# Kernel optimization log

Hardware: AMD Instinct MI355X
Metric: run time of the kernel (lower is better)

Reference implementation:

```python
import jax, jax.numpy as jnp
import numpy as np

NQ = 8  # qubits per circuit (= d_k = n_qubits_ffn)
# Fixed realization of tq.RandomLayer(n_ops=8): 6 parametric rotations + 2 CNOTs
OPS = [("ry", 0), ("rx", 3), ("rz", 5), ("cx", (1, 4)), ("ry", 6), ("rx", 2), ("cx", (0, 7)), ("rz", 4)]
_CNOT = jnp.asarray(np.array([[1,0,0,0],[0,1,0,0],[0,0,0,1],[0,0,1,0]], dtype=np.complex64).reshape(2,2,2,2))
# signs[i, w] = +1 if bit of wire w in basis index i is 0, else -1 (PauliZ eigenvalue)
_idx = np.arange(2 ** NQ)
_bits = (_idx[:, None] >> (NQ - 1 - np.arange(NQ))) & 1
SIGNS = jnp.asarray((1 - 2 * _bits).astype(np.float32))

def _rot(kind, t):
    c = jnp.cos(t / 2).astype(jnp.complex64)
    s = jnp.sin(t / 2).astype(jnp.complex64)
    z = jnp.zeros_like(c)
    if kind == "rx":
        return jnp.stack([jnp.stack([c, -1j * s]), jnp.stack([-1j * s, c])])
    if kind == "ry":
        return jnp.stack([jnp.stack([c, -s]), jnp.stack([s, c])])
    tc = t.astype(jnp.complex64)
    return jnp.stack([jnp.stack([jnp.exp(-1j * tc / 2), z]), jnp.stack([z, jnp.exp(1j * tc / 2)])])

def _apply1(state, U, w):
    st = jnp.tensordot(U, state, axes=((1,), (w + 1,)))
    return jnp.moveaxis(st, 0, w + 1)

def _apply2(state, c, t):  # CNOT, requires c < t (true for OPS)
    st = jnp.tensordot(_CNOT, state, axes=((2, 3), (c + 1, t + 1)))
    return jnp.moveaxis(st, (0, 1), (c + 1, t + 1))

def qcircuit(angles, thetas):
    """angles: [N, NQ] data angles (RX encoding); thetas: [6] gate params.
    Returns PauliZ expectations [N, NQ] (float32)."""
    N = angles.shape[0]
    c = jnp.cos(angles / 2)
    s = jnp.sin(angles / 2)
    amp = jnp.stack([c.astype(jnp.complex64), (-1j) * s.astype(jnp.complex64)], axis=-1)  # [N, NQ, 2]
    # RX-encoded product state |psi> = prod_w RX(x_w)|0>
    state = amp[:, 0]
    for w in range(1, NQ):
        state = state[..., None] * amp[:, w].reshape((N,) + (1,) * w + (2,))
    pi = 0
    for kind, arg in OPS:
        if kind == "cx":
            state = _apply2(state, *arg)
        else:
            state = _apply1(state, _rot(kind, thetas[pi]), arg)
            pi += 1
    probs = jnp.abs(state.reshape(N, -1)) ** 2  # [N, 2^NQ]
    return probs @ SIGNS  # [N, NQ]

def _ln(x, g, b, eps=1e-5):
    m = x.mean(-1, keepdims=True)
    v = ((x - m) ** 2).mean(-1, keepdims=True)
    return (x - m) / jnp.sqrt(v + eps) * g + b

def setup_inputs() -> dict:
    key = jax.random.key(0)
    ks = jax.random.split(key, 8)
    B, S, E, FF = 4, 1024, 64, 256
    return {
        "x": jax.random.normal(ks[0], (B, S, E), dtype=jnp.float32),
        "attn_theta": jax.random.uniform(ks[1], (6,), dtype=jnp.float32, maxval=2 * np.pi),
        "Wc": jax.random.normal(ks[2], (E, E), dtype=jnp.float32) * 0.1,
        "bc": jnp.zeros((E,), jnp.float32),
        "g1": jnp.ones((E,), jnp.float32),
        "beta1": jnp.zeros((E,), jnp.float32),
        "ffn_theta": jax.random.uniform(ks[3], (6,), dtype=jnp.float32, maxval=2 * np.pi),
        "W1": jax.random.normal(ks[4], (NQ, FF), dtype=jnp.float32) * 0.3,
        "b1": jnp.zeros((FF,), jnp.float32),
        "W2": jax.random.normal(ks[5], (FF, E), dtype=jnp.float32) * 0.06,
        "b2": jnp.zeros((E,), jnp.float32),
        "g2": jnp.ones((E,), jnp.float32),
        "beta2": jnp.zeros((E,), jnp.float32),
    }

def reference(x, attn_theta, Wc, bc, g1, beta1, ffn_theta, W1, b1, W2, b2, g2, beta2):
    B, S, E = x.shape
    dk = NQ  # d_k = embed_dim // num_heads = 8
    # --- quantum multi-head attention (same qlayer shared across heads -> vectorize) ---
    q = qcircuit(x.reshape(B * S * (E // dk), dk), attn_theta)  # [B*S*H, dk]
    attn = q.reshape(B, S, E) @ Wc + bc
    y = _ln(x + attn, g1, beta1)
    # --- quantum FFN: encoder uses first NQ features of each token ---
    qf = qcircuit(y.reshape(B * S, E)[:, :NQ], ffn_theta)  # [B*S, NQ]
    h = jax.nn.relu(qf @ W1 + b1)
    ffn = (h @ W2 + b2).reshape(B, S, E)
    return _ln(y + ffn, g2, beta2)
```

## Files before the change

### kernel.cpp

```cpp
#include <hip/hip_runtime.h>


typedef _Float16 h2f  __attribute__((ext_vector_type(2)));
typedef _Float16 f16x8 __attribute__((ext_vector_type(8)));
typedef float    f32x4 __attribute__((ext_vector_type(4)));

__device__ __forceinline__ int pk(float a, float b) {
    return __builtin_bit_cast(int, __builtin_amdgcn_cvt_pkrtz(a, b));
}
__device__ __forceinline__ float fdot2i(int a, int b, float c) {
    return __builtin_amdgcn_fdot2(__builtin_bit_cast(h2f, a),
                                  __builtin_bit_cast(h2f, b), c, false);
}
__device__ __forceinline__ float rl_f(float v, int l) {
    return __int_as_float(__builtin_amdgcn_readlane(__float_as_int(v), l));
}
__device__ __forceinline__ int rl_i(int v, int l) {
    return __builtin_amdgcn_readlane(v, l);
}
__device__ __forceinline__ void wave_sum2(float& a, float& b) {
#pragma unroll
    for (int m = 32; m > 0; m >>= 1) {
        a += __shfl_xor(a, m, 64);
        b += __shfl_xor(b, m, 64);
    }
}

__global__ __launch_bounds__(512, 2)
void qtb_fused8(const float* __restrict__ x,
                const float* __restrict__ th_a,
                const float* __restrict__ Wc,
                const float* __restrict__ bc,
                const float* __restrict__ g1,
                const float* __restrict__ be1,
                const float* __restrict__ th_f,
                const float* __restrict__ W1,
                const float* __restrict__ b1,
                const float* __restrict__ W2,
                const float* __restrict__ b2,
                const float* __restrict__ g2,
                const float* __restrict__ be2,
                float* __restrict__ out)
{
    __shared__ __align__(16) int2      sWc[16 * 64];
    __shared__ __align__(16) int4      sW1[256];
    __shared__ __align__(16) _Float16  sW2t[64][264];
    __shared__ __align__(16) _Float16  sH[16][264];
    __shared__ __align__(16) float     sO[16][66];

    const int tid  = threadIdx.x;
    const int lane = tid & 63;
    const int wv   = tid >> 6;
    const int w    = lane & 7;
    const int gb   = lane & ~7;
    const int tok0 = (blockIdx.x * 8 + wv) * 2;

    {
        int k0 = (tid & 31) * 8;
        int e0 = (tid >> 5) * 4;
        float4 r[8];
#pragma unroll
        for (int i = 0; i < 8; ++i)
            r[i] = *(const float4*)&W2[(k0 + i) * 64 + e0];
        const float* f = (const float*)r;
#pragma unroll
        for (int j = 0; j < 4; ++j) {
            int4 wj = make_int4(pk(f[0 * 4 + j], f[1 * 4 + j]),
                                pk(f[2 * 4 + j], f[3 * 4 + j]),
                                pk(f[4 * 4 + j], f[5 * 4 + j]),
                                pk(f[6 * 4 + j], f[7 * 4 + j]));
            *(int4*)&sW2t[e0 + j][k0] = wj;
        }
    }
    if (tid < 256) {
        int q2 = tid >> 4;
        int e0 = (tid & 15) * 4;
        const float* b = Wc + e0;
        float4 r0 = *(const float4*)&b[(2 * q2     ) * 64];
        float4 r1 = *(const float4*)&b[(2 * q2 +  1) * 64];
        float4 r2 = *(const float4*)&b[(2 * q2 + 32) * 64];
        float4 r3 = *(const float4*)&b[(2 * q2 + 33) * 64];
        int4* dst = (int4*)&sWc[q2 * 64 + e0];
        dst[0] = make_int4(pk(r0.x, r2.x), pk(r1.x, r3.x),
                           pk(r0.y, r2.y), pk(r1.y, r3.y));
        dst[1] = make_int4(pk(r0.z, r2.z), pk(r1.z, r3.z),
                           pk(r0.w, r2.w), pk(r1.w, r3.w));
    } else if (tid < 320) {
        int j0 = (tid - 256) * 4;
        float4 r[8];
#pragma unroll
        for (int k = 0; k < 8; ++k) r[k] = *(const float4*)&W1[k * 256 + j0];
        const float* f = (const float*)r;
        int4* dst = &sW1[j0];
#pragma unroll
        for (int j = 0; j < 4; ++j)
            dst[j] = make_int4(pk(f[0 * 4 + j], f[4 * 4 + j]),
                               pk(f[1 * 4 + j], f[5 * 4 + j]),
                               pk(f[2 * 4 + j], f[6 * 4 + j]),
                               pk(f[3 * 4 + j], f[7 * 4 + j]));
    }

    float xr[2];
#pragma unroll
    for (int t = 0; t < 2; ++t) xr[t] = x[(tok0 + t) * 64 + lane];

    const float C0a = __cosf(th_a[0]);
    const float T1a = th_a[1];
    const float C3a = __cosf(th_a[3]);
    const float T4a = th_a[4];
    const float C0f = __cosf(th_f[0]);
    const float T1f = th_f[1];
    const float C3f = __cosf(th_f[3]);
    const float T4f = th_f[4];

    const float bcL = bc[lane], g1L = g1[lane], be1L = be1[lane];
    const float b2L = b2[lane], g2L = g2[lane], be2L = be2[lane];
    float b1L[4];
#pragma unroll
    for (int r = 0; r < 4; ++r) b1L[r] = b1[r * 64 + lane];

    const float dA = (w == 2) ? T4a : ((w == 3) ? T1a : 0.0f);
    int zp[2];
#pragma unroll
    for (int t = 0; t < 2; ++t) {
        float c  = __cosf(xr[t] + dA);
        float c0 = __shfl(c, gb, 64);
        float c1 = __shfl(c, gb + 1, 64);
        float zz = c * ((w == 0) ? C0a : ((w == 6) ? C3a : 1.0f));
        if (w == 4) zz = c * c1;
        if (w == 7) zz = C0a * c0 * c;
        zp[t] = pk(zz, __shfl_xor(zz, 32, 64));
    }

    __syncthreads();

    float acc[2] = {bcL, bcL};
#pragma unroll 4
    for (int q2 = 0; q2 < 16; ++q2) {
        int2 wq = sWc[q2 * 64 + lane];
        int q = 2 * q2;
        acc[0] = fdot2i(rl_i(zp[0], q),     wq.x, acc[0]);
        acc[1] = fdot2i(rl_i(zp[1], q),     wq.x, acc[1]);
        acc[0] = fdot2i(rl_i(zp[0], q + 1), wq.y, acc[0]);
        acc[1] = fdot2i(rl_i(zp[1], q + 1), wq.y, acc[1]);
    }

    float y[2];
#pragma unroll
    for (int t = 0; t < 2; ++t) {
        float v = xr[t] + acc[t];
        float s = v, s2 = v * v;
        wave_sum2(s, s2);
        float m   = s * 0.015625f;
        float var = s2 * 0.015625f - m * m;
        y[t] = (v - m) * rsqrtf(var + 1e-5f) * g1L + be1L;
    }

    int4 w1q[4];
#pragma unroll
    for (int r = 0; r < 4; ++r) w1q[r] = sW1[r * 64 + lane];

    const float dF = (w == 2) ? T4f : ((w == 3) ? T1f : 0.0f);
#pragma unroll
    for (int t = 0; t < 2; ++t) {
        float cy = __cosf(y[t] + dF);
        float c0 = rl_f(cy, 0);
        float c1 = rl_f(cy, 1);
        float qz = cy * ((w == 0) ? C0f : ((w == 6) ? C3f : 1.0f));
        if (w == 4) qz = cy * c1;
        if (w == 7) qz = C0f * c0 * cy;
        int qp0 = pk(rl_f(qz, 0), rl_f(qz, 4));
        int qp1 = pk(rl_f(qz, 1), rl_f(qz, 5));
        int qp2 = pk(rl_f(qz, 2), rl_f(qz, 6));
        int qp3 = pk(rl_f(qz, 3), rl_f(qz, 7));
#pragma unroll
        for (int r = 0; r < 4; ++r) {
            float a = b1L[r];
            a = fdot2i(qp0, w1q[r].x, a);
            a = fdot2i(qp1, w1q[r].y, a);
            a = fdot2i(qp2, w1q[r].z, a);
            a = fdot2i(qp3, w1q[r].w, a);
            sH[wv * 2 + t][r * 64 + lane] = (_Float16)fmaxf(a, 0.0f);
        }
    }

    __syncthreads();

    if (wv < 4) {
        const int col = lane & 15;
        const int kg  = lane >> 4;
        f32x4 cacc = {0.0f, 0.0f, 0.0f, 0.0f};
#pragma unroll
        for (int ks = 0; ks < 8; ++ks) {
            f16x8 af = *(const f16x8*)&sH[col][ks * 32 + kg * 8];
            f16x8 bf = *(const f16x8*)&sW2t[wv * 16 + col][ks * 32 + kg * 8];
            cacc = __builtin_amdgcn_mfma_f32_16x16x32_f16(af, bf, cacc, 0, 0, 0);
        }
#pragma unroll
        for (int r = 0; r < 4; ++r)
            sO[kg * 4 + r][wv * 16 + col] = cacc[r];
    }

    __syncthreads();

#pragma unroll
    for (int t = 0; t < 2; ++t) {
        float v = y[t] + b2L + sO[wv * 2 + t][lane];
        float s = v, s2 = v * v;
        wave_sum2(s, s2);
        float m   = s * 0.015625f;
        float var = s2 * 0.015625f - m * m;
        out[(tok0 + t) * 64 + lane] = (v - m) * rsqrtf(var + 1e-5f) * g2L + be2L;
    }
}

extern "C" void kernel_launch(void* const* d_in, const int* in_sizes, int n_in,
                              void* d_out, int out_size, void* d_ws, size_t ws_size,
                              hipStream_t stream)
{
    const float* x   = (const float*)d_in[0];
    const float* at  = (const float*)d_in[1];
    const float* Wc  = (const float*)d_in[2];
    const float* bcp = (const float*)d_in[3];
    const float* g1  = (const float*)d_in[4];
    const float* be1 = (const float*)d_in[5];
    const float* ft  = (const float*)d_in[6];
    const float* W1  = (const float*)d_in[7];
    const float* b1  = (const float*)d_in[8];
    const float* W2  = (const float*)d_in[9];
    const float* b2  = (const float*)d_in[10];
    const float* g2  = (const float*)d_in[11];
    const float* be2 = (const float*)d_in[12];
    float* out = (float*)d_out;

    qtb_fused8<<<256, 512, 0, stream>>>(x, at, Wc, bcp, g1, be1, ft,
                                        W1, b1, W2, b2, g2, be2, out);
}
```

Before: 11.58 us.

## Compute attention projection with MFMA and prefetch W2 fragments on idle waves

The per-lane readlane/fdot2 loop for the Wc projection is replaced by a 16x16x32 f16 MFMA over a transposed Wc tile in shared memory. Quantum Z outputs are staged through shared memory for this, which adds a barrier. Waves 4-7 now preload their W2 B-fragments into registers while waves 0-3 do the attention MFMA, and later those same waves run the FFN MFMA. The result is an extra sync and shared round trip in exchange for less scalar dot-product work, at the cost of higher register pressure.

```diff
diff --git a/kernel.cpp b/kernel.cpp
--- a/kernel.cpp
+++ b/kernel.cpp
@@ -1,7 +1,7 @@
 #include <hip/hip_runtime.h>
 
 
-typedef _Float16 h2f  __attribute__((ext_vector_type(2)));
+typedef _Float16 h2f   __attribute__((ext_vector_type(2)));
 typedef _Float16 f16x8 __attribute__((ext_vector_type(8)));
 typedef float    f32x4 __attribute__((ext_vector_type(4)));
 
@@ -15,9 +15,6 @@
 __device__ __forceinline__ float rl_f(float v, int l) {
     return __int_as_float(__builtin_amdgcn_readlane(__float_as_int(v), l));
 }
-__device__ __forceinline__ int rl_i(int v, int l) {
-    return __builtin_amdgcn_readlane(v, l);
-}
 __device__ __forceinline__ void wave_sum2(float& a, float& b) {
 #pragma unroll
     for (int m = 32; m > 0; m >>= 1) {
@@ -27,7 +24,7 @@
 }
 
 __global__ __launch_bounds__(512, 2)
-void qtb_fused8(const float* __restrict__ x,
+void qtb_fused9(const float* __restrict__ x,
                 const float* __restrict__ th_a,
                 const float* __restrict__ Wc,
                 const float* __restrict__ bc,
@@ -42,9 +39,11 @@
                 const float* __restrict__ be2,
                 float* __restrict__ out)
 {
-    __shared__ __align__(16) int2      sWc[16 * 64];
+    __shared__ __align__(16) _Float16  sWct[64][72];
     __shared__ __align__(16) int4      sW1[256];
     __shared__ __align__(16) _Float16  sW2t[64][264];
+    __shared__ __align__(16) _Float16  sZ[16][72];
+    __shared__ __align__(16) float     sA[16][66];
     __shared__ __align__(16) _Float16  sH[16][264];
     __shared__ __align__(16) float     sO[16][66];
 
@@ -54,6 +53,7 @@
     const int w    = lane & 7;
     const int gb   = lane & ~7;
     const int tok0 = (blockIdx.x * 8 + wv) * 2;
+    const int tl   = wv * 2;
 
     {
         int k0 = (tid & 31) * 8;
@@ -64,40 +64,40 @@
             r[i] = *(const float4*)&W2[(k0 + i) * 64 + e0];
         const float* f = (const float*)r;
 #pragma unroll
-        for (int j = 0; j < 4; ++j) {
-            int4 wj = make_int4(pk(f[0 * 4 + j], f[1 * 4 + j]),
-                                pk(f[2 * 4 + j], f[3 * 4 + j]),
-                                pk(f[4 * 4 + j], f[5 * 4 + j]),
-                                pk(f[6 * 4 + j], f[7 * 4 + j]));
-            *(int4*)&sW2t[e0 + j][k0] = wj;
-        }
-    }
-    if (tid < 256) {
-        int q2 = tid >> 4;
-        int e0 = (tid & 15) * 4;
-        const float* b = Wc + e0;
-        float4 r0 = *(const float4*)&b[(2 * q2     ) * 64];
-        float4 r1 = *(const float4*)&b[(2 * q2 +  1) * 64];
-        float4 r2 = *(const float4*)&b[(2 * q2 + 32) * 64];
-        float4 r3 = *(const float4*)&b[(2 * q2 + 33) * 64];
-        int4* dst = (int4*)&sWc[q2 * 64 + e0];
-        dst[0] = make_int4(pk(r0.x, r2.x), pk(r1.x, r3.x),
-                           pk(r0.y, r2.y), pk(r1.y, r3.y));
-        dst[1] = make_int4(pk(r0.z, r2.z), pk(r1.z, r3.z),
-                           pk(r0.w, r2.w), pk(r1.w, r3.w));
-    } else if (tid < 320) {
-        int j0 = (tid - 256) * 4;
+        for (int j = 0; j < 4; ++j)
+            *(int4*)&sW2t[e0 + j][k0] =
+                make_int4(pk(f[0 * 4 + j], f[1 * 4 + j]),
+                          pk(f[2 * 4 + j], f[3 * 4 + j]),
+                          pk(f[4 * 4 + j], f[5 * 4 + j]),
+                          pk(f[6 * 4 + j], f[7 * 4 + j]));
+    }
+    if (tid < 128) {
+        int q0 = (tid & 7) * 8;
+        int e0 = (tid >> 3) * 4;
+        float4 r[8];
+#pragma unroll
+        for (int i = 0; i < 8; ++i)
+            r[i] = *(const float4*)&Wc[(q0 + i) * 64 + e0];
+        const float* f = (const float*)r;
+#pragma unroll
+        for (int j = 0; j < 4; ++j)
+            *(int4*)&sWct[e0 + j][q0] =
+                make_int4(pk(f[0 * 4 + j], f[1 * 4 + j]),
+                          pk(f[2 * 4 + j], f[3 * 4 + j]),
+                          pk(f[4 * 4 + j], f[5 * 4 + j]),
+                          pk(f[6 * 4 + j], f[7 * 4 + j]));
+    } else if (tid < 192) {
+        int j0 = (tid - 128) * 4;
         float4 r[8];
 #pragma unroll
         for (int k = 0; k < 8; ++k) r[k] = *(const float4*)&W1[k * 256 + j0];
         const float* f = (const float*)r;
-        int4* dst = &sW1[j0];
 #pragma unroll
         for (int j = 0; j < 4; ++j)
-            dst[j] = make_int4(pk(f[0 * 4 + j], f[4 * 4 + j]),
-                               pk(f[1 * 4 + j], f[5 * 4 + j]),
-                               pk(f[2 * 4 + j], f[6 * 4 + j]),
-                               pk(f[3 * 4 + j], f[7 * 4 + j]));
+            sW1[j0 + j] = make_int4(pk(f[0 * 4 + j], f[4 * 4 + j]),
+                                    pk(f[1 * 4 + j], f[5 * 4 + j]),
+                                    pk(f[2 * 4 + j], f[6 * 4 + j]),
+                                    pk(f[3 * 4 + j], f[7 * 4 + j]));
     }
 
     float xr[2];
@@ -120,7 +120,6 @@
     for (int r = 0; r < 4; ++r) b1L[r] = b1[r * 64 + lane];
 
     const float dA = (w == 2) ? T4a : ((w == 3) ? T1a : 0.0f);
-    int zp[2];
 #pragma unroll
     for (int t = 0; t < 2; ++t) {
         float c  = __cosf(xr[t] + dA);
@@ -129,26 +128,40 @@
         float zz = c * ((w == 0) ? C0a : ((w == 6) ? C3a : 1.0f));
         if (w == 4) zz = c * c1;
         if (w == 7) zz = C0a * c0 * c;
-        zp[t] = pk(zz, __shfl_xor(zz, 32, 64));
-    }
-
-    __syncthreads();
-
-    float acc[2] = {bcL, bcL};
-#pragma unroll 4
-    for (int q2 = 0; q2 < 16; ++q2) {
-        int2 wq = sWc[q2 * 64 + lane];
-        int q = 2 * q2;
-        acc[0] = fdot2i(rl_i(zp[0], q),     wq.x, acc[0]);
-        acc[1] = fdot2i(rl_i(zp[1], q),     wq.x, acc[1]);
-        acc[0] = fdot2i(rl_i(zp[0], q + 1), wq.y, acc[0]);
-        acc[1] = fdot2i(rl_i(zp[1], q + 1), wq.y, acc[1]);
-    }
+        sZ[tl + t][lane] = (_Float16)zz;
+    }
+
+    __syncthreads();
+
+    const int col = lane & 15;
+    const int kg  = lane >> 4;
+
+    f16x8 bf2[8];
+    if (wv >= 4) {
+#pragma unroll
+        for (int ks = 0; ks < 8; ++ks)
+            bf2[ks] = *(const f16x8*)&sW2t[(wv - 4) * 16 + col][ks * 32 + kg * 8];
+    }
+
+    if (wv < 4) {
+        f32x4 cacc = {0.0f, 0.0f, 0.0f, 0.0f};
+#pragma unroll
+        for (int ks = 0; ks < 2; ++ks) {
+            f16x8 af = *(const f16x8*)&sZ[col][ks * 32 + kg * 8];
+            f16x8 bf = *(const f16x8*)&sWct[wv * 16 + col][ks * 32 + kg * 8];
+            cacc = __builtin_amdgcn_mfma_f32_16x16x32_f16(af, bf, cacc, 0, 0, 0);
+        }
+#pragma unroll
+        for (int r = 0; r < 4; ++r)
+            sA[kg * 4 + r][wv * 16 + col] = cacc[r];
+    }
+
+    __syncthreads();
 
     float y[2];
 #pragma unroll
     for (int t = 0; t < 2; ++t) {
-        float v = xr[t] + acc[t];
+        float v = xr[t] + sA[tl + t][lane] + bcL;
         float s = v, s2 = v * v;
         wave_sum2(s, s2);
         float m   = s * 0.015625f;
@@ -180,32 +193,29 @@
             a = fdot2i(qp1, w1q[r].y, a);
             a = fdot2i(qp2, w1q[r].z, a);
             a = fdot2i(qp3, w1q[r].w, a);
-            sH[wv * 2 + t][r * 64 + lane] = (_Float16)fmaxf(a, 0.0f);
+            sH[tl + t][r * 64 + lane] = (_Float16)fmaxf(a, 0.0f);
         }
     }
 
     __syncthreads();
 
-    if (wv < 4) {
-        const int col = lane & 15;
-        const int kg  = lane >> 4;
+    if (wv >= 4) {
         f32x4 cacc = {0.0f, 0.0f, 0.0f, 0.0f};
 #pragma unroll
         for (int ks = 0; ks < 8; ++ks) {
             f16x8 af = *(const f16x8*)&sH[col][ks * 32 + kg * 8];
-            f16x8 bf = *(const f16x8*)&sW2t[wv * 16 + col][ks * 32 + kg * 8];
-            cacc = __builtin_amdgcn_mfma_f32_16x16x32_f16(af, bf, cacc, 0, 0, 0);
+            cacc = __builtin_amdgcn_mfma_f32_16x16x32_f16(af, bf2[ks], cacc, 0, 0, 0);
         }
 #pragma unroll
         for (int r = 0; r < 4; ++r)
-            sO[kg * 4 + r][wv * 16 + col] = cacc[r];
-    }
-
-    __syncthreads();
-
-#pragma unroll
-    for (int t = 0; t < 2; ++t) {
-        float v = y[t] + b2L + sO[wv * 2 + t][lane];
+            sO[kg * 4 + r][(wv - 4) * 16 + col] = cacc[r];
+    }
+
+    __syncthreads();
+
+#pragma unroll
+    for (int t = 0; t < 2; ++t) {
+        float v = y[t] + b2L + sO[tl + t][lane];
         float s = v, s2 = v * v;
         wave_sum2(s, s2);
         float m   = s * 0.015625f;
@@ -233,6 +243,6 @@
     const float* be2 = (const float*)d_in[12];
     float* out = (float*)d_out;
 
-    qtb_fused8<<<256, 512, 0, stream>>>(x, at, Wc, bcp, g1, be1, ft,
+    qtb_fused9<<<256, 512, 0, stream>>>(x, at, Wc, bcp, g1, be1, ft,
                                         W1, b1, W2, b2, g2, be2, out);
 }
```

After: 11.40 us. Within noise of the previous version (-1.5%).
